# Kernel optimization log

Measured on AMD Instinct MI355X. Metric: run time of the kernel, lower is better.

## Reference

```python
import jax, jax.numpy as jnp
import numpy as np
from jax import lax

D = 300   # dim (hidden_size)
T = 1024  # grown history length
B = 128   # batched independent steps


def _conv(x, w, b):
    # NCHW conv, 3x3, stride 1, SAME padding (matches nn.Conv2d(.,.,3,1,1))
    return lax.conv_general_dilated(x, w, (1, 1), 'SAME',
                                    dimension_numbers=('NCHW', 'OIHW', 'NCHW')) + b[None, :, None, None]


def _bn(x, g, b, eps=1e-5):
    # eval-mode BatchNorm2d with running_mean=0, running_var=1
    return x * (g / jnp.sqrt(1.0 + eps))[None, :, None, None] + b[None, :, None, None]


def setup_inputs():
    key = jax.random.key(0)
    ks = iter(jax.random.split(key, 64))
    def rn(shape, scale=1.0):
        return jax.random.normal(next(ks), shape, dtype=jnp.float32) * scale
    inp = {
        'x': rn((B, D)),
        'hidden_states': rn((B, T, D)),
        'past_ht': rn((B, T, D)),
        'past_c': rn((B, T, D)),
        'W': rn((4 * D, 2 * D), 0.05),
        'b': rn((4 * D,)).at[:D].set(1.0),   # self.b[:dim] = 1
        'W_h': rn((10, D), 0.1),
        'W_x': rn((10, D), 0.1),
        'W_ht': rn((10, D), 0.1),
        'v': rn((10,)),
        'rb_w': rn((1600, 4 * D), 0.02),  # reshape_bef: Linear(1200, 1600)
        'rb_b': rn((1600,), 0.02),
        'rp_w': rn((4 * D, 1600), 0.02),  # reshape_pos: Linear(1600, 1200)
        'rp_b': rn((4 * D,), 0.02),
    }
    chans = [(1, 32), (32, 64), (64, 64), (64, 64), (64, 32), (32, 1)]
    for i, (ci, co) in enumerate(chans, 1):
        inp[f'c{i}_w'] = rn((co, ci, 3, 3), 0.1)
        inp[f'c{i}_b'] = rn((co,), 0.02)
        inp[f'c{i}_g'] = jnp.ones((co,), jnp.float32)
        inp[f'c{i}_beta'] = jnp.zeros((co,), jnp.float32)
    inp['pc_w'] = rn((1, 2, 3, 3), 0.1)
    inp['pc_b'] = rn((1,), 0.02)
    inp['pc_g'] = jnp.ones((1,), jnp.float32)
    inp['pc_beta'] = jnp.zeros((1,), jnp.float32)
    return inp


def reference(x, hidden_states, past_ht, past_c, W, b, W_h, W_x, W_ht, v,
              rb_w, rb_b, rp_w, rp_b,
              c1_w, c1_b, c1_g, c1_beta, c2_w, c2_b, c2_g, c2_beta,
              c3_w, c3_b, c3_g, c3_beta, c4_w, c4_b, c4_g, c4_beta,
              c5_w, c5_b, c5_g, c5_beta, c6_w, c6_b, c6_g, c6_beta,
              pc_w, pc_b, pc_g, pc_beta):
    # --- intra-attention over the grown history (vectorized over k) ---
    # a_k = v @ tanh(W_h h_k + W_x x + W_ht pht_k)
    e = jnp.tanh(jnp.einsum('btd,kd->btk', hidden_states, W_h)
                 + jnp.einsum('bd,kd->bk', x, W_x)[:, None, :]
                 + jnp.einsum('btd,kd->btk', past_ht, W_ht))
    s = jax.nn.softmax(jnp.einsum('btk,k->bt', e, v), axis=-1)
    ht = jnp.einsum('bt,btd->bd', s, hidden_states)
    ct = jnp.einsum('bt,btd->bd', s, past_c)
    # --- gate pre-activations ---
    whx = jnp.concatenate([ht, x], axis=-1) @ W.T + b          # [B, 1200]
    whx = whx @ rb_w.T + rb_b                                  # [B, 1600]
    pre = whx.reshape(-1, 1, 40, 40)
    # --- inter conv block (dropout is identity in eval) ---
    y = pre
    for (w, bi, g, be) in ((c1_w, c1_b, c1_g, c1_beta), (c2_w, c2_b, c2_g, c2_beta),
                           (c3_w, c3_b, c3_g, c3_beta), (c4_w, c4_b, c4_g, c4_beta),
                           (c5_w, c5_b, c5_g, c5_beta), (c6_w, c6_b, c6_g, c6_beta)):
        y = _bn(jax.nn.relu(_conv(y, w, bi)), g, be)
    y = _bn(_conv(jnp.concatenate([pre, y], axis=1), pc_w, pc_b), pc_g, pc_beta)
    whx = y.reshape(-1, 1600) @ rp_w.T + rp_b                  # [B, 1200]
    # --- LSTM gating ---
    f_t = jax.nn.sigmoid(whx[:, :D])
    o_t = jax.nn.sigmoid(whx[:, D:2 * D])
    i_t = jax.nn.sigmoid(whx[:, 2 * D:3 * D])
    ch_t = jnp.tanh(whx[:, 3 * D:4 * D])
    c = f_t * ct + i_t * ch_t
    h = o_t * jnp.tanh(c)
    return h
```

## Files before the change

### kernel.cpp

```cpp
#include <hip/hip_runtime.h>
#include <hip/hip_bf16.h>
#include <cstdint>
#include <cstddef>

typedef unsigned short u16;
typedef unsigned int u32;

#define DEV __device__ __forceinline__

DEV float bf2f(u16 u){ union{unsigned int i; float f;} c; c.i = ((unsigned)u)<<16; return c.f; }
DEV u16 f2bf(float f){ union{float f;unsigned int i;} c; c.f=f; unsigned int r = c.i + 0x7FFFu + ((c.i>>16)&1u); return (u16)(r>>16); }
DEV unsigned int pk2(float a, float b){
  __hip_bfloat162 t = __float22bfloat162_rn(float2{a,b});
  union { __hip_bfloat162 h; unsigned int u; } cv; cv.h = t; return cv.u;
}

typedef __attribute__((ext_vector_type(8))) short bf16x8;
typedef __attribute__((ext_vector_type(4))) float f32x4;
typedef __attribute__((ext_vector_type(8))) unsigned short us8v;

static constexpr size_t OFF_XW    = 0;
static constexpr size_t OFF_WHX2  = 8192;
static constexpr size_t OFF_WHX3  = OFF_WHX2 + (size_t)128*1600*4;
static constexpr size_t OFF_W21   = OFF_WHX3 + (size_t)128*1200*4;
static constexpr size_t OFF_WB2   = OFF_W21  + (size_t)288*4;
static constexpr size_t OFF_WB3   = OFF_WB2  + (size_t)18432*2;
static constexpr size_t OFF_WB4   = OFF_WB3  + (size_t)36864*2;
static constexpr size_t OFF_WB5   = OFF_WB4  + (size_t)36864*2;
static constexpr size_t OFF_W26   = OFF_WB5  + (size_t)18432*2;
static constexpr size_t OFF_PAR   = OFF_W26  + (size_t)288*4;
static constexpr size_t OFF_WPACK = OFF_PAR  + (size_t)6*768;
static constexpr size_t OFF_WB1G  = OFF_WPACK+ (size_t)20480*2;
static constexpr size_t OFF_RBWB  = OFF_WB1G + (size_t)1216*608*2;
static constexpr size_t OFF_RPWB  = OFF_RBWB + (size_t)1600*1216*2;
static constexpr size_t OFF_CAT   = OFF_RPWB + (size_t)1216*1600*2;
static constexpr size_t OFF_WHX1B = OFF_CAT  + (size_t)128*608*2;
static constexpr size_t OFF_O16B  = OFF_WHX1B+ (size_t)128*1216*2;
static constexpr size_t OFF_CT    = OFF_O16B + (size_t)128*1600*2;
static constexpr size_t OFF_A32   = OFF_CT   + (size_t)128*300*4;
static constexpr size_t OFF_B64   = OFF_A32  + (size_t)128*1764*32*2;
static constexpr size_t OFF_C64   = OFF_B64  + (size_t)128*1764*64*2;
static constexpr size_t OFF_P0    = OFF_C64  + (size_t)128*1764*64*2;
static constexpr size_t OFF_Y6    = OFF_P0   + (size_t)128*1764*2;
static constexpr size_t OFF_PARTX = OFF_Y6   + (size_t)128*1764*2;
static constexpr size_t OFF_END   = OFF_PARTX+ (size_t)128*32*608*4;

DEV void ring0(u16* buf, int j){
  int b = j/164, i = j%164;
  int y, x;
  if      (i < 42){ y = 0;        x = i; }
  else if (i < 84){ y = 41;       x = i-42; }
  else if (i < 124){ y = i-84+1;  x = 0; }
  else             { y = i-124+1; x = 41; }
  buf[(size_t)b*1764 + y*42 + x] = 0;
}
DEV void bzero(u16* buf, int j, int CH, int C){
  int c8 = j % CH; int rem = j / CH;
  int i = rem % 164, b = rem / 164;
  int y, x;
  if      (i < 42){ y = 0;        x = i; }
  else if (i < 84){ y = 41;       x = i-42; }
  else if (i < 124){ y = i-84+1;  x = 0; }
  else             { y = i-124+1; x = 41; }
  us8v z = {0,0,0,0,0,0,0,0};
  *(us8v*)(buf + ((size_t)b*1764 + y*42 + x)*C + c8*8) = z;
}
DEV void cvW(const float* w, u16* dst, size_t j, int CI){
  int ci = j % CI; size_t rem = j / CI; int dydx = rem % 9; int co = rem / 9;
  dst[j] = f2bf(w[((size_t)co*CI + ci)*9 + dydx]);
}

__global__ __launch_bounds__(256) void prep_k(const float* __restrict__ Wh, const float* __restrict__ Wht,
    const float* __restrict__ x, const float* __restrict__ Wx,
    u16* __restrict__ wp, float* __restrict__ xw){
  int bid = blockIdx.x, tid = threadIdx.x;
  if (bid < 80){
    int j = bid*256 + tid;
    int jj = j&7, col=(j>>3)&15, kg=(j>>7)&3, rest=j>>9;
    int ks = rest%10, tz = rest/10;
    int k = ks*32 + kg*8 + jj;
    const float* src = tz ? Wht : Wh;
    wp[j] = f2bf((col<10 && k<300)? src[col*300+k] : 0.f);
  } else {
    int gw = (bid-80)*4 + (tid>>6);
    int lane = tid & 63;
    int b = gw/10, k = gw%10;
    float a = 0.f;
    for (int d = lane; d < 300; d += 64)
      a = fmaf(x[b*300+d], Wx[k*300+d], a);
    #pragma unroll
    for (int off=1; off<64; off<<=1) a += __shfl_xor(a, off);
    if (lane==0) xw[b*16+k] = a;
  }
}

struct MArgs {
  const float *hs, *pht, *pc, *v, *xw;
  const u16* wpack;
  float* part;
  const float* cw0; const float* cw1; const float* cw2; const float* cw3; const float* cw4; const float* cw5;
  const float* cb[6]; const float* cg[6]; const float* cbe[6];
  const float* Wg; const float* rbw; const float* rpw;
  float* w21; float* w26; float* par;
  u16 *wb2, *wb3, *wb4, *wb5, *Wb1, *rbwb, *rpwb;
  u16 *p0, *y6, *catb, *A32, *B64, *C64;
};
__global__ __launch_bounds__(256,3) void attn_mega(MArgs a){
  int bid = blockIdx.x;
  int tid = threadIdx.x;
  if (bid < 4096){
    __shared__ u16 HL[32][328];
    __shared__ u16 PL[32][328];
    __shared__ float PS[2][32][18];
    __shared__ float PP[32];
    __shared__ float ML[2];
    int chunk = bid & 31, b = bid >> 5;
    int rr0 = (b<<10) + chunk*32;
    const float* hsrc = a.hs  + (size_t)rr0*300;
    const float* psrc = a.pht + (size_t)rr0*300;
    const float* csrc = a.pc  + (size_t)rr0*300;
    float4 creg[10];
    #pragma unroll
    for (int rnd=0; rnd<10; rnd++){
      int idx = rnd*256 + tid;
      if (idx < 2400) creg[rnd] = *(const float4*)(csrc + idx*4);
    }
    #pragma unroll
    for (int rnd=0; rnd<10; rnd++){
      int idx = rnd*256 + tid;
      if (idx < 2400){
        float4 qh = *(const float4*)(hsrc + idx*4);
        float4 qp = *(const float4*)(psrc + idx*4);
        int row = idx/75, colp = (idx - row*75)*4;
        uint2 pvh; pvh.x = pk2(qh.x,qh.y); pvh.y = pk2(qh.z,qh.w);
        uint2 pvp; pvp.x = pk2(qp.x,qp.y); pvp.y = pk2(qp.z,qp.w);
        *(uint2*)(&HL[row][colp]) = pvh;
        *(uint2*)(&PL[row][colp]) = pvp;
      }
    }
    #pragma unroll
    for (int j=0;j<2;j++){
      int idx = j*256 + tid;
      if (idx < 448){
        int row = idx/14, cc = 300 + (idx - row*14)*2;
        *(u32*)(&HL[row][cc]) = 0u;
        *(u32*)(&PL[row][cc]) = 0u;
      }
    }
    __syncthreads();
    {
      int w = tid>>6, l = tid&63;
      int c = l&15, g = l>>4;
      int tz = w>>1, rf = w&1;
      const u16 (*SL)[328] = tz ? PL : HL;
      const u16* wbase = a.wpack + (size_t)tz*5120;
      f32x4 acc = (f32x4){0.f,0.f,0.f,0.f};
      #pragma unroll
      for (int ks=0; ks<10; ks++){
        bf16x8 af  = *(const bf16x8*)(&SL[rf*16 + c][ks*32 + g*8]);
        bf16x8 bfr = *(const bf16x8*)(wbase + ((ks*4 + g)*16 + c)*8);
        acc = __builtin_amdgcn_mfma_f32_16x16x32_bf16(af, bfr, acc, 0, 0, 0);
      }
      #pragma unroll
      for (int r=0;r<4;r++) PS[tz][rf*16 + g*4 + r][c] = acc[r];
    }
    __syncthreads();
    #pragma unroll
    for (int rnd=0; rnd<10; rnd++){
      int idx = rnd*256 + tid;
      if (idx < 2400){
        int row = idx/75, colp = (idx - row*75)*4;
        uint2 pv; pv.x = pk2(creg[rnd].x, creg[rnd].y); pv.y = pk2(creg[rnd].z, creg[rnd].w);
        *(uint2*)(&PL[row][colp]) = pv;
      }
    }
    if (tid < 32){
      float s = 0.f;
      #pragma unroll
      for (int k=0;k<10;k++)
        s += a.v[k]*tanhf(PS[0][tid][k] + PS[1][tid][k] + a.xw[b*16+k]);
      float m = s;
      #pragma unroll
      for (int off=1; off<32; off<<=1) m = fmaxf(m, __shfl_xor(m, off));
      float p = expf(s - m);
      float l = p;
      #pragma unroll
      for (int off=1; off<32; off<<=1) l += __shfl_xor(l, off);
      PP[tid] = p;
      if (tid==0){ ML[0]=m; ML[1]=l; }
    }
    __syncthreads();
    float* pp = a.part + ((size_t)b*32 + chunk)*608;
    if (tid < 150){
      int d = tid*2;
      float h0=0,h1=0,c0=0,c1=0;
      #pragma unroll
      for (int t=0;t<32;t++){
        float p = PP[t];
        u32 hw = *(const u32*)(&HL[t][d]);
        u32 cw = *(const u32*)(&PL[t][d]);
        h0 = fmaf(p, bf2f((u16)hw),       h0);
        h1 = fmaf(p, bf2f((u16)(hw>>16)), h1);
        c0 = fmaf(p, bf2f((u16)cw),       c0);
        c1 = fmaf(p, bf2f((u16)(cw>>16)), c1);
      }
      *(float2*)(pp + 4 + d)   = float2{h0,h1};
      *(float2*)(pp + 308 + d) = float2{c0,c1};
    }
    if (tid==0){ pp[0]=ML[0]; pp[1]=ML[1]; }
  } else if (bid < 5901){
    int zid = (bid-4096)*256 + tid;
    if (zid < 20992) ring0(a.p0, zid);
    else if (zid < 41984) ring0(a.y6, zid-20992);
    else if (zid < 42112){
      int b = zid - 41984;
      us8v z = {0,0,0,0,0,0,0,0};
      *(us8v*)(a.catb + (size_t)b*608 + 600) = z;
    }
    else if (zid < 126080){ bzero(a.A32, zid-42112, 4, 32); }
    else if (zid < 294016){ bzero(a.B64, zid-126080, 8, 64); }
    else if (zid < 461952){ bzero(a.C64, zid-294016, 8, 64); }
  } else {
    const float isc = 1.0f/sqrtf(1.00001f);
    const float* cwA[6] = {a.cw0,a.cw1,a.cw2,a.cw3,a.cw4,a.cw5};
    for (size_t id = (size_t)(bid-5901)*256 + tid; id < 4742467ull; id += (size_t)512*256){
      if (id < 288){
        int co = id % 32; size_t rem = id / 32; int k = rem % 9;
        a.w21[id] = cwA[0][co*9 + k];
      } else if (id < 18720){ cvW(cwA[1], a.wb2, id-288, 32); }
      else if (id < 55584){ cvW(cwA[2], a.wb3, id-18720, 64); }
      else if (id < 92448){ cvW(cwA[3], a.wb4, id-55584, 64); }
      else if (id < 110880){ cvW(cwA[4], a.wb5, id-92448, 64); }
      else if (id < 111168){
        size_t j = id - 110880;
        a.w26[j] = cwA[5][j];
      } else if (id < 850496){
        size_t j = id - 111168; int k = (int)(j % 608); int n = (int)(j / 608);
        a.Wb1[j] = f2bf((n<1200 && k<600)? a.Wg[(size_t)n*600+k] : 0.f);
      } else if (id < 2796096){
        size_t j = id - 850496; int k = (int)(j % 1216); int n = (int)(j / 1216);
        a.rbwb[j] = f2bf((k<1200)? a.rbw[(size_t)n*1200+k] : 0.f);
      } else if (id < 4741696){
        size_t j = id - 2796096; int k = (int)(j % 1600); int n = (int)(j / 1600);
        a.rpwb[j] = f2bf((n<1200)? a.rpw[(size_t)n*1600+k] : 0.f);
      } else {
        size_t j = id - 4741696;
        int ci, CO; size_t base;
        if (j < 96){ ci=0; CO=32; base=0; }
        else if (j < 288){ ci=1; CO=64; base=96; }
        else if (j < 480){ ci=2; CO=64; base=288; }
        else if (j < 672){ ci=3; CO=64; base=480; }
        else if (j < 768){ ci=4; CO=32; base=672; }
        else { ci=5; CO=1; base=768; }
        size_t jj = j - base; int t = (int)(jj / CO); int c = (int)(jj % CO);
        float* p = a.par + (size_t)ci*192;
        p[t*CO + c] = (t==0)? a.cb[ci][c] : (t==1)? a.cg[ci][c]*isc : a.cbe[ci][c];
      }
    }
  }
}

__global__ __launch_bounds__(192) void attn_reduce(const float* __restrict__ part,
    const float* __restrict__ x, float* __restrict__ ct, u16* __restrict__ catb){
  int b = blockIdx.x;
  int tid = threadIdx.x;
  const float* pb = part + (size_t)b*32*608;
  float M = -3.0e38f;
  #pragma unroll
  for (int j=0;j<32;j++) M = fmaxf(M, pb[j*608]);
  float L = 0.f;
  #pragma unroll
  for (int j=0;j<32;j++) L += pb[j*608+1]*expf(pb[j*608]-M);
  if (tid < 150){
    int d = tid*2;
    float a0=0,a1=0,b0=0,b1=0;
    #pragma unroll
    for (int j=0;j<32;j++){
      float w = expf(pb[j*608]-M);
      float2 hh = *(const float2*)(pb + j*608 + 4 + d);
      float2 cc = *(const float2*)(pb + j*608 + 308 + d);
      a0 = fmaf(w,hh.x,a0); a1 = fmaf(w,hh.y,a1);
      b0 = fmaf(w,cc.x,b0); b1 = fmaf(w,cc.y,b1);
    }
    float inv = 1.f/L;
    *(float2*)(ct + (size_t)b*300 + d) = float2{b0*inv, b1*inv};
    *(u32*)(catb + (size_t)b*608 + d)       = pk2(a0*inv, a1*inv);
    *(u32*)(catb + (size_t)b*608 + 300 + d) = pk2(x[(size_t)b*300 + d], x[(size_t)b*300 + d + 1]);
  }
}

template<int KP, int OMODE>
__global__ __launch_bounds__(256) void gemm_mfma(int NW, int NB, int ldo,
    const u16* __restrict__ inB, const u16* __restrict__ Wb,
    const float* __restrict__ bias, void* __restrict__ outp){
  __shared__ float red[4][64][4];
  int w = threadIdx.x>>6, l = threadIdx.x&63;
  int c = l&15, g = l>>4;
  int n0 = blockIdx.x*16;
  int b0 = blockIdx.y*16;
  const u16* arow = Wb  + (size_t)(n0 + c)*KP + g*8;
  const u16* brow = inB + (size_t)(b0 + c)*KP + g*8;
  f32x4 acc = (f32x4){0.f,0.f,0.f,0.f};
  for (int ks = w; ks < KP/32; ks += 4){
    bf16x8 af = *(const bf16x8*)(arow + ks*32);
    bf16x8 bf = *(const bf16x8*)(brow + ks*32);
    acc = __builtin_amdgcn_mfma_f32_16x16x32_bf16(af, bf, acc, 0, 0, 0);
  }
  #pragma unroll
  for (int r=0;r<4;r++) red[w][l][r] = acc[r];
  __syncthreads();
  if (w==0){
    float s0 = red[0][l][0]+red[1][l][0]+red[2][l][0]+red[3][l][0];
    float s1 = red[0][l][1]+red[1][l][1]+red[2][l][1]+red[3][l][1];
    float s2 = red[0][l][2]+red[1][l][2]+red[2][l][2]+red[3][l][2];
    float s3 = red[0][l][3]+red[1][l][3]+red[2][l][3]+red[3][l][3];
    int b = b0 + c, nb = n0 + g*4;
    if (nb < NW){
      float4 bi;
      if (nb < NB) bi = *(const float4*)(bias + nb);
      else { bi.x=0; bi.y=0; bi.z=0; bi.w=0; }
      float o0=s0+bi.x, o1=s1+bi.y, o2=s2+bi.z, o3=s3+bi.w;
      if (OMODE==2){
        int row = nb/40, col = nb%40;
        u16* pp0 = (u16*)outp + (size_t)b*1764 + (row+1)*42 + (col+1);
        pp0[0]=f2bf(o0); pp0[1]=f2bf(o1); pp0[2]=f2bf(o2); pp0[3]=f2bf(o3);
      } else if (OMODE==1){
        ushort4 st; st.x=f2bf(o0); st.y=f2bf(o1); st.z=f2bf(o2); st.w=f2bf(o3);
        *(ushort4*)((u16*)outp + (size_t)b*ldo + nb) = st;
      } else {
        float4 st; st.x=o0; st.y=o1; st.z=o2; st.w=o3;
        *(float4*)((float*)outp + (size_t)b*ldo + nb) = st;
      }
    }
  }
}

template<int CI, int CO>
__global__ __launch_bounds__(256) void conv_tile(const u16* __restrict__ in, u16* __restrict__ out,
    const u16* __restrict__ wB, const float* __restrict__ par){
  constexpr int PCI  = CI + 8;
  constexpr int MF   = CO/16;
  constexpr int FPW  = MF;
  constexpr int KC   = CI/32;
  constexpr int KROW = CI*9;
  constexpr int CH8  = CI/8;
  __shared__ u16 TIN[100*PCI];
  int tile = blockIdx.x;
  int b = blockIdx.y;
  int y0 = (tile/5)*8, x0 = (tile%5)*8;
  const u16* inb = in + (size_t)b*1764*CI;
  for (int g = threadIdx.x; g < 100*CH8; g += 256){
    int pix = g/CH8, ch = g - pix*CH8;
    int r = pix/10, cc = pix - r*10;
    us8v vdat = *(const us8v*)(inb + ((size_t)(y0+r)*42 + (x0+cc))*CI + ch*8);
    *(us8v*)(&TIN[pix*PCI + ch*8]) = vdat;
  }
  __syncthreads();
  int w = threadIdx.x>>6, l = threadIdx.x&63;
  int c = l&15, kg = l>>4;
  int mg, f0;
  if (MF==4){ mg = w; f0 = 0; } else { mg = w&1; f0 = (w>>1)*2; }
  int pxb[FPW];
  #pragma unroll
  for (int fi=0; fi<FPW; fi++){
    int px = (f0+fi)*16 + c;
    int ty = px>>3, tx = px&7;
    pxb[fi] = (ty*10 + tx)*PCI + kg*8;
  }
  const u16* wrow = wB + (size_t)(mg*16 + c)*KROW;
  f32x4 acc[FPW];
  #pragma unroll
  for (int fi=0; fi<FPW; fi++) acc[fi] = (f32x4){0.f,0.f,0.f,0.f};
  #pragma unroll
  for (int dy=0;dy<3;dy++)
  #pragma unroll
  for (int dx=0;dx<3;dx++){
    int dydx = dy*3+dx;
    #pragma unroll
    for (int kc=0; kc<KC; kc++){
      bf16x8 af = *(const bf16x8*)(wrow + dydx*CI + kc*32 + kg*8);
      #pragma unroll
      for (int fi=0; fi<FPW; fi++){
        bf16x8 bf = *(const bf16x8*)(&TIN[pxb[fi] + (dy*10+dx)*PCI + kc*32]);
        acc[fi] = __builtin_amdgcn_mfma_f32_16x16x32_bf16(af, bf, acc[fi], 0, 0, 0);
      }
    }
  }
  u16* ob = out + (size_t)b*1764*CO;
  int co0 = mg*16 + kg*4;
  const float4 bia = *(const float4*)(par + co0);
  const float4 sc  = *(const float4*)(par + CO + co0);
  const float4 be  = *(const float4*)(par + 2*CO + co0);
  #pragma unroll
  for (int fi=0; fi<FPW; fi++){
    int px = (f0+fi)*16 + c;
    int y = y0 + (px>>3), x = x0 + (px&7);
    ushort4 s;
    s.x = f2bf(fmaxf(acc[fi][0]+bia.x,0.f)*sc.x + be.x);
    s.y = f2bf(fmaxf(acc[fi][1]+bia.y,0.f)*sc.y + be.y);
    s.z = f2bf(fmaxf(acc[fi][2]+bia.z,0.f)*sc.z + be.z);
    s.w = f2bf(fmaxf(acc[fi][3]+bia.w,0.f)*sc.w + be.w);
    *(ushort4*)(ob + (size_t)((y+1)*42 + (x+1))*CO + co0) = s;
  }
}

template<int CI, int CO, bool TT>
__global__ __launch_bounds__(256) void conv_main(const u16* __restrict__ in, u16* __restrict__ out,
    const float* __restrict__ w2, const float* __restrict__ par){
  int b = blockIdx.x;
  int wave = threadIdx.x >> 6;
  int lane = threadIdx.x & 63;
  int tile, co;
  if (TT){ tile = blockIdx.y*8 + wave*2 + (lane>>5); co = lane & 31; }
  else   { tile = blockIdx.y*4 + wave;               co = lane; }
  int y0 = (tile >> 3)*5, x0 = (tile & 7)*5;
  const u16* inb = in + (size_t)b*1764*CI;
  float acc[25];
  #pragma unroll
  for (int p=0;p<25;p++) acc[p]=0.f;
  for (int ci=0; ci<CI; ci++){
    float win[49];
    #pragma unroll
    for (int r=0;r<7;r++)
      #pragma unroll
      for (int c=0;c<7;c++)
        win[r*7+c] = bf2f(inb[ ((y0+r)*42 + (x0+c))*CI + ci ]);
    float wk[9];
    #pragma unroll
    for (int k=0;k<9;k++) wk[k] = w2[(ci*9+k)*CO + co];
    #pragma unroll
    for (int py=0;py<5;py++)
      #pragma unroll
      for (int px=0;px<5;px++){
        float s = acc[py*5+px];
        #pragma unroll
        for (int dy=0;dy<3;dy++)
          #pragma unroll
          for (int dx=0;dx<3;dx++)
            s = fmaf(wk[dy*3+dx], win[(py+dy)*7 + (px+dx)], s);
        acc[py*5+px] = s;
      }
  }
  float bia = par[co], sc = par[CO+co], be = par[2*CO+co];
  u16* outb = out + (size_t)b*1764*CO;
  #pragma unroll
  for (int py=0;py<5;py++)
    #pragma unroll
    for (int px=0;px<5;px++){
      float vv = fmaxf(acc[py*5+px] + bia, 0.f)*sc + be;
      outb[ ((y0+py+1)*42 + (x0+px+1))*CO + co ] = f2bf(vv);
    }
}

__global__ __launch_bounds__(256) void conv_c6(const u16* __restrict__ in, u16* __restrict__ y6,
    const float* __restrict__ w6, const float* __restrict__ par6){
  int id = blockIdx.x*256 + threadIdx.x;
  int b = id/1600, p = id%1600;
  int y = p/40, x = p%40;
  const u16* inb = in + (size_t)b*1764*32;
  float acc = 0.f;
  #pragma unroll
  for (int dy=0;dy<3;dy++)
    #pragma unroll
    for (int dx=0;dx<3;dx++){
      const u16* q = inb + ((y+dy)*42 + (x+dx))*32;
      int k = dy*3+dx;
      #pragma unroll
      for (int g=0; g<4; g++){
        us8v vv8 = *(const us8v*)(q + g*8);
        #pragma unroll
        for (int j=0;j<8;j++)
          acc = fmaf(w6[(g*8+j)*9 + k], bf2f(vv8[j]), acc);
      }
    }
  float vv = fmaxf(acc + par6[0], 0.f)*par6[1] + par6[2];
  y6[(size_t)b*1764 + (y+1)*42 + (x+1)] = f2bf(vv);
}

__global__ __launch_bounds__(256) void conv_pc(const u16* __restrict__ p0, const u16* __restrict__ y6,
    const float* __restrict__ pcw, const float* __restrict__ pcb,
    const float* __restrict__ pcg, const float* __restrict__ pcbe,
    u16* __restrict__ o16b){
  int id = blockIdx.x*256 + threadIdx.x;
  int b = id/1600, p = id%1600;
  int y = p/40, x = p%40;
  float acc = 0.f;
  #pragma unroll
  for (int dy=0;dy<3;dy++)
    #pragma unroll
    for (int dx=0;dx<3;dx++){
      size_t o = (size_t)b*1764 + (y+dy)*42 + (x+dx);
      acc = fmaf(pcw[dy*3+dx],     bf2f(p0[o]), acc);
      acc = fmaf(pcw[9 + dy*3+dx], bf2f(y6[o]), acc);
    }
  float sc = pcg[0] * (1.0f/sqrtf(1.00001f));
  o16b[id] = f2bf((acc + pcb[0])*sc + pcbe[0]);
}

__global__ __launch_bounds__(256) void gate_k(const float* __restrict__ whx3, const float* __restrict__ ct,
                                              float* __restrict__ outp){
  int id = blockIdx.x*256 + threadIdx.x;
  if (id >= 38400) return;
  int b = id/300, d = id%300;
  const float* r = whx3 + (size_t)b*1200;
  float ft = 1.f/(1.f+expf(-r[d]));
  float ot = 1.f/(1.f+expf(-r[300+d]));
  float it = 1.f/(1.f+expf(-r[600+d]));
  float ch = tanhf(r[900+d]);
  float c  = ft*ct[id] + it*ch;
  outp[id] = ot*tanhf(c);
}

extern "C" void kernel_launch(void* const* d_in, const int* in_sizes, int n_in,
                              void* d_out, int out_size, void* d_ws, size_t ws_size,
                              hipStream_t stream){
  const float* x    = (const float*)d_in[0];
  const float* hs   = (const float*)d_in[1];
  const float* pht  = (const float*)d_in[2];
  const float* pc   = (const float*)d_in[3];
  const float* W    = (const float*)d_in[4];
  const float* bb   = (const float*)d_in[5];
  const float* Wh   = (const float*)d_in[6];
  const float* Wx   = (const float*)d_in[7];
  const float* Wht  = (const float*)d_in[8];
  const float* v    = (const float*)d_in[9];
  const float* rbw  = (const float*)d_in[10];
  const float* rbb  = (const float*)d_in[11];
  const float* rpw  = (const float*)d_in[12];
  const float* rpb  = (const float*)d_in[13];
  const float *cw[6], *cb[6], *cg[6], *cbe[6];
  for (int i=0;i<6;i++){
    cw[i]=(const float*)d_in[14+4*i]; cb[i]=(const float*)d_in[15+4*i];
    cg[i]=(const float*)d_in[16+4*i]; cbe[i]=(const float*)d_in[17+4*i];
  }
  const float* pcw = (const float*)d_in[38];
  const float* pcb = (const float*)d_in[39];
  const float* pcg = (const float*)d_in[40];
  const float* pcbe= (const float*)d_in[41];

  char* ws = (char*)d_ws;
  float* xw    = (float*)(ws + OFF_XW);
  float* whx3  = (float*)(ws + OFF_WHX3);
  float* w21   = (float*)(ws + OFF_W21);
  u16*   wb2   = (u16*)  (ws + OFF_WB2);
  u16*   wb3   = (u16*)  (ws + OFF_WB3);
  u16*   wb4   = (u16*)  (ws + OFF_WB4);
  u16*   wb5   = (u16*)  (ws + OFF_WB5);
  float* w26   = (float*)(ws + OFF_W26);
  u16*   wpack = (u16*)  (ws + OFF_WPACK);
  u16*   wb1g  = (u16*)  (ws + OFF_WB1G);
  u16*   rbwb  = (u16*)  (ws + OFF_RBWB);
  u16*   rpwb  = (u16*)  (ws + OFF_RPWB);
  u16*   catb  = (u16*)  (ws + OFF_CAT);
  u16*   whx1b = (u16*)  (ws + OFF_WHX1B);
  u16*   o16b  = (u16*)  (ws + OFF_O16B);
  float* part  = (float*)(ws + OFF_PARTX);
  float* parb  = (float*)(ws + OFF_PAR);
  float* ct = (float*)(ws + OFF_CT);
  u16* A32 = (u16*)(ws + OFF_A32);
  u16* B64 = (u16*)(ws + OFF_B64);
  u16* C64 = (u16*)(ws + OFF_C64);
  u16* P0  = (u16*)(ws + OFF_P0);
  u16* Y6  = (u16*)(ws + OFF_Y6);

  MArgs ma;
  ma.hs=hs; ma.pht=pht; ma.pc=pc; ma.v=v; ma.xw=xw; ma.wpack=wpack; ma.part=part;
  ma.cw0=cw[0]; ma.cw1=cw[1]; ma.cw2=cw[2]; ma.cw3=cw[3]; ma.cw4=cw[4]; ma.cw5=cw[5];
  for (int i=0;i<6;i++){ ma.cb[i]=cb[i]; ma.cg[i]=cg[i]; ma.cbe[i]=cbe[i]; }
  ma.Wg=W; ma.rbw=rbw; ma.rpw=rpw;
  ma.w21=w21; ma.w26=w26; ma.par=parb;
  ma.wb2=wb2; ma.wb3=wb3; ma.wb4=wb4; ma.wb5=wb5;
  ma.Wb1=wb1g; ma.rbwb=rbwb; ma.rpwb=rpwb;
  ma.p0=P0; ma.y6=Y6; ma.catb=catb; ma.A32=A32; ma.B64=B64; ma.C64=C64;

  prep_k<<<400,256,0,stream>>>(Wh, Wht, x, Wx, wpack, xw);
  attn_mega<<<6413,256,0,stream>>>(ma);
  attn_reduce<<<128,192,0,stream>>>(part, x, ct, catb);

  gemm_mfma< 608,1><<<dim3(76,8), 256,0,stream>>>(1216, 1200, 1216, catb,  wb1g, bb,  whx1b);
  gemm_mfma<1216,2><<<dim3(100,8),256,0,stream>>>(1600, 1600, 0,    whx1b, rbwb, rbb, P0);

  conv_main<1,32,true><<<dim3(128,8),256,0,stream>>>(P0, A32, w21, parb);
  conv_tile<32,64><<<dim3(25,128),256,0,stream>>>(A32, B64, wb2, parb + 192);
  conv_tile<64,64><<<dim3(25,128),256,0,stream>>>(B64, C64, wb3, parb + 384);
  conv_tile<64,64><<<dim3(25,128),256,0,stream>>>(C64, B64, wb4, parb + 576);
  conv_tile<64,32><<<dim3(25,128),256,0,stream>>>(B64, A32, wb5, parb + 768);
  conv_c6<<<800,256,0,stream>>>(A32, Y6, w26, parb + 960);
  conv_pc<<<800,256,0,stream>>>(P0, Y6, pcw, pcb, pcg, pcbe, o16b);

  gemm_mfma<1600,0><<<dim3(75,8),256,0,stream>>>(1200, 1200, 1200, o16b, rpwb, rpb, whx3);
  gate_k<<<150,256,0,stream>>>(whx3, ct, (float*)d_out);
}
```

Baseline: 352.9 us.

## Use 32x32x16 MFMA conv kernel for 64-channel layers and fuse conv6 with pc conv

Adds a conv_t32 kernel that computes each 8x8 spatial tile with 32x32x16 bf16 MFMA instructions, loading weights straight from global memory and input from a padded LDS tile. It replaces the three 64-output-channel conv_tile launches. Separately, conv_c6 and conv_pc are merged into one tiled kernel that computes the 1-channel conv6 output with a halo into LDS and then applies the pc conv. This removes the Y6 intermediate and one launch, at the cost of recomputing halo pixels and running only 100 of 128 threads.

```diff
diff --git a/kernel.cpp b/kernel.cpp
--- a/kernel.cpp
+++ b/kernel.cpp
@@ -17,6 +17,7 @@
 
 typedef __attribute__((ext_vector_type(8))) short bf16x8;
 typedef __attribute__((ext_vector_type(4))) float f32x4;
+typedef __attribute__((ext_vector_type(16))) float f32x16;
 typedef __attribute__((ext_vector_type(8))) unsigned short us8v;
 
 static constexpr size_t OFF_XW    = 0;
@@ -335,6 +336,63 @@
   }
 }
 
+template<int CI>
+__global__ __launch_bounds__(256) void conv_t32(const u16* __restrict__ in, u16* __restrict__ out,
+    const u16* __restrict__ wB, const float* __restrict__ par){
+  constexpr int PCI  = CI + 8;
+  constexpr int K16  = CI/16;
+  constexpr int KROW = CI*9;
+  constexpr int CH8  = CI/8;
+  __shared__ u16 TIN[100*PCI];
+  int tile = blockIdx.x;
+  int b = blockIdx.y;
+  int y0 = (tile/5)*8, x0 = (tile%5)*8;
+  const u16* inb = in + (size_t)b*1764*CI;
+  for (int g = threadIdx.x; g < 100*CH8; g += 256){
+    int pix = g/CH8, ch = g - pix*CH8;
+    int r = pix/10, cc = pix - r*10;
+    us8v vdat = *(const us8v*)(inb + ((size_t)(y0+r)*42 + (x0+cc))*CI + ch*8);
+    *(us8v*)(&TIN[pix*PCI + ch*8]) = vdat;
+  }
+  __syncthreads();
+  int w = threadIdx.x>>6, l = threadIdx.x&63;
+  int mg = w & 1, pg = w >> 1;
+  int pl = l & 31, kh = l >> 5;
+  int px = pg*32 + pl;
+  int ty = px>>3, tx = px&7;
+  int pxb = (ty*10 + tx)*PCI + kh*8;
+  const u16* wrow = wB + (size_t)(mg*32 + pl)*KROW + kh*8;
+  f32x16 acc;
+  #pragma unroll
+  for (int i=0;i<16;i++) acc[i] = 0.f;
+  #pragma unroll
+  for (int dy=0;dy<3;dy++)
+  #pragma unroll
+  for (int dx=0;dx<3;dx++){
+    int dydx = dy*3+dx;
+    #pragma unroll
+    for (int kc=0; kc<K16; kc++){
+      bf16x8 af = *(const bf16x8*)(wrow + dydx*CI + kc*16);
+      bf16x8 bf = *(const bf16x8*)(&TIN[pxb + (dy*10+dx)*PCI + kc*16]);
+      acc = __builtin_amdgcn_mfma_f32_32x32x16_bf16(af, bf, acc, 0, 0, 0);
+    }
+  }
+  u16* ob = out + (size_t)b*1764*64 + (size_t)((y0+ty+1)*42 + (x0+tx+1))*64;
+  #pragma unroll
+  for (int rg=0; rg<4; rg++){
+    int co0 = mg*32 + rg*8 + kh*4;
+    const float4 bia = *(const float4*)(par + co0);
+    const float4 sc  = *(const float4*)(par + 64 + co0);
+    const float4 be  = *(const float4*)(par + 128 + co0);
+    ushort4 s;
+    s.x = f2bf(fmaxf(acc[rg*4+0]+bia.x,0.f)*sc.x + be.x);
+    s.y = f2bf(fmaxf(acc[rg*4+1]+bia.y,0.f)*sc.y + be.y);
+    s.z = f2bf(fmaxf(acc[rg*4+2]+bia.z,0.f)*sc.z + be.z);
+    s.w = f2bf(fmaxf(acc[rg*4+3]+bia.w,0.f)*sc.w + be.w);
+    *(ushort4*)(ob + co0) = s;
+  }
+}
+
 template<int CI, int CO>
 __global__ __launch_bounds__(256) void conv_tile(const u16* __restrict__ in, u16* __restrict__ out,
     const u16* __restrict__ wB, const float* __restrict__ par){
@@ -452,49 +510,58 @@
     }
 }
 
-__global__ __launch_bounds__(256) void conv_c6(const u16* __restrict__ in, u16* __restrict__ y6,
-    const float* __restrict__ w6, const float* __restrict__ par6){
-  int id = blockIdx.x*256 + threadIdx.x;
-  int b = id/1600, p = id%1600;
-  int y = p/40, x = p%40;
-  const u16* inb = in + (size_t)b*1764*32;
-  float acc = 0.f;
-  #pragma unroll
-  for (int dy=0;dy<3;dy++)
-    #pragma unroll
-    for (int dx=0;dx<3;dx++){
-      const u16* q = inb + ((y+dy)*42 + (x+dx))*32;
-      int k = dy*3+dx;
-      #pragma unroll
-      for (int g=0; g<4; g++){
-        us8v vv8 = *(const us8v*)(q + g*8);
-        #pragma unroll
-        for (int j=0;j<8;j++)
-          acc = fmaf(w6[(g*8+j)*9 + k], bf2f(vv8[j]), acc);
-      }
-    }
-  float vv = fmaxf(acc + par6[0], 0.f)*par6[1] + par6[2];
-  y6[(size_t)b*1764 + (y+1)*42 + (x+1)] = f2bf(vv);
-}
-
-__global__ __launch_bounds__(256) void conv_pc(const u16* __restrict__ p0, const u16* __restrict__ y6,
+__global__ __launch_bounds__(128) void conv_tail(const u16* __restrict__ A32, const u16* __restrict__ p0,
+    const float* __restrict__ w6, const float* __restrict__ par6,
     const float* __restrict__ pcw, const float* __restrict__ pcb,
     const float* __restrict__ pcg, const float* __restrict__ pcbe,
     u16* __restrict__ o16b){
-  int id = blockIdx.x*256 + threadIdx.x;
-  int b = id/1600, p = id%1600;
-  int y = p/40, x = p%40;
-  float acc = 0.f;
-  #pragma unroll
-  for (int dy=0;dy<3;dy++)
-    #pragma unroll
-    for (int dx=0;dx<3;dx++){
-      size_t o = (size_t)b*1764 + (y+dy)*42 + (x+dx);
-      acc = fmaf(pcw[dy*3+dx],     bf2f(p0[o]), acc);
-      acc = fmaf(pcw[9 + dy*3+dx], bf2f(y6[o]), acc);
-    }
-  float sc = pcg[0] * (1.0f/sqrtf(1.00001f));
-  o16b[id] = f2bf((acc + pcb[0])*sc + pcbe[0]);
+  __shared__ float YT[10][10];
+  __shared__ float PT[10][10];
+  int tile = blockIdx.x, b = blockIdx.y;
+  int ty0 = (tile/5)*8, tx0 = (tile%5)*8;
+  int tid = threadIdx.x;
+  if (tid < 100){
+    int iy = tid/10, ix = tid%10;
+    int Y = ty0 + iy, X = tx0 + ix;
+    float yv = 0.f;
+    if (Y>=1 && Y<=40 && X>=1 && X<=40){
+      const u16* inb = A32 + (size_t)b*1764*32;
+      float acc = 0.f;
+      #pragma unroll
+      for (int dy=0;dy<3;dy++)
+        #pragma unroll
+        for (int dx=0;dx<3;dx++){
+          const u16* q = inb + ((size_t)(Y-1+dy)*42 + (X-1+dx))*32;
+          int k = dy*3+dx;
+          #pragma unroll
+          for (int g=0; g<4; g++){
+            us8v v8 = *(const us8v*)(q + g*8);
+            #pragma unroll
+            for (int j=0;j<8;j++)
+              acc = fmaf(w6[(g*8+j)*9 + k], bf2f(v8[j]), acc);
+          }
+        }
+      yv = fmaxf(acc + par6[0], 0.f)*par6[1] + par6[2];
+    }
+    YT[iy][ix] = yv;
+    PT[iy][ix] = bf2f(p0[(size_t)b*1764 + Y*42 + X]);
+  }
+  __syncthreads();
+  if (tid < 64){
+    int oy = tid>>3, ox = tid&7;
+    float acc = 0.f;
+    #pragma unroll
+    for (int dy=0;dy<3;dy++)
+      #pragma unroll
+      for (int dx=0;dx<3;dx++){
+        int k = dy*3+dx;
+        acc = fmaf(pcw[k],   PT[oy+dy][ox+dx], acc);
+        acc = fmaf(pcw[9+k], YT[oy+dy][ox+dx], acc);
+      }
+    float scv = pcg[0] * (1.0f/sqrtf(1.00001f));
+    int y = ty0+oy, x = tx0+ox;
+    o16b[(size_t)b*1600 + y*40 + x] = f2bf((acc + pcb[0])*scv + pcbe[0]);
+  }
 }
 
 __global__ __launch_bounds__(256) void gate_k(const float* __restrict__ whx3, const float* __restrict__ ct,
@@ -581,12 +648,11 @@
   gemm_mfma<1216,2><<<dim3(100,8),256,0,stream>>>(1600, 1600, 0,    whx1b, rbwb, rbb, P0);
 
   conv_main<1,32,true><<<dim3(128,8),256,0,stream>>>(P0, A32, w21, parb);
-  conv_tile<32,64><<<dim3(25,128),256,0,stream>>>(A32, B64, wb2, parb + 192);
-  conv_tile<64,64><<<dim3(25,128),256,0,stream>>>(B64, C64, wb3, parb + 384);
-  conv_tile<64,64><<<dim3(25,128),256,0,stream>>>(C64, B64, wb4, parb + 576);
+  conv_t32<32><<<dim3(25,128),256,0,stream>>>(A32, B64, wb2, parb + 192);
+  conv_t32<64><<<dim3(25,128),256,0,stream>>>(B64, C64, wb3, parb + 384);
+  conv_t32<64><<<dim3(25,128),256,0,stream>>>(C64, B64, wb4, parb + 576);
   conv_tile<64,32><<<dim3(25,128),256,0,stream>>>(B64, A32, wb5, parb + 768);
-  conv_c6<<<800,256,0,stream>>>(A32, Y6, w26, parb + 960);
-  conv_pc<<<800,256,0,stream>>>(P0, Y6, pcw, pcb, pcg, pcbe, o16b);
+  conv_tail<<<dim3(25,128),128,0,stream>>>(A32, P0, w26, parb + 960, pcw, pcb, pcg, pcbe, o16b);
 
   gemm_mfma<1600,0><<<dim3(75,8),256,0,stream>>>(1200, 1200, 1200, o16b, rpwb, rpb, whx3);
   gate_k<<<150,256,0,stream>>>(whx3, ct, (float*)d_out);
```

Measured after the change: 416.9 us. 18.1% more time.
